# Kernel tuning notes

Hardware: AMD Instinct MI355X
Metric: run time of the kernel (lower is better)

Reference implementation:

```python
import jax, jax.numpy as jnp
import numpy as np

BN_EPS = 1e-5


def _conv_bn_elu(x, w, b, bn_scale, bn_bias, bn_mean, bn_var):
    # 1x1 conv == channel-mixing matmul: x [B,C,H,W], w [O,C]
    y = jnp.einsum('bchw,oc->bohw', x, w) + b[None, :, None, None]
    inv = bn_scale * jax.lax.rsqrt(bn_var + BN_EPS)
    y = y * inv[None, :, None, None] + (bn_bias - bn_mean * inv)[None, :, None, None]
    return jax.nn.elu(y)


def setup_inputs() -> dict:
    key = jax.random.key(0)
    ks = jax.random.split(key, 24)
    B, C, H, W = 4, 128, 64, 64
    d = {}
    d['x_q'] = jax.random.normal(ks[0], (B, C, H, W), jnp.float32)
    d['x_k'] = jax.random.normal(ks[1], (B, C, H, W), jnp.float32)
    d['x_v'] = jax.random.normal(ks[2], (B, C, H, W), jnp.float32)
    scale = 1.0 / np.sqrt(C)
    i = 3
    for p in ('q', 'k', 'v'):
        d[f'{p}_w'] = jax.random.normal(ks[i], (C, C), jnp.float32) * scale; i += 1
        d[f'{p}_b'] = jax.random.normal(ks[i], (C,), jnp.float32) * 0.01; i += 1
        d[f'{p}_bn_scale'] = jnp.ones((C,), jnp.float32) + 0.1 * jax.random.normal(ks[i], (C,), jnp.float32); i += 1
        d[f'{p}_bn_bias'] = 0.1 * jax.random.normal(ks[i], (C,), jnp.float32); i += 1
        d[f'{p}_bn_mean'] = 0.1 * jax.random.normal(ks[i], (C,), jnp.float32); i += 1
        d[f'{p}_bn_var'] = jax.random.uniform(ks[i], (C,), jnp.float32, 0.5, 1.5); i += 1
    # torch inits gamma/beta to zero; use small nonzero values so output is informative
    d['gamma'] = jnp.array([0.5], jnp.float32)
    d['beta'] = jnp.array([0.5], jnp.float32)
    return d


def reference(x_q, x_k, x_v,
              q_w, q_b, q_bn_scale, q_bn_bias, q_bn_mean, q_bn_var,
              k_w, k_b, k_bn_scale, k_bn_bias, k_bn_mean, k_bn_var,
              v_w, v_b, v_bn_scale, v_bn_bias, v_bn_mean, v_bn_var,
              gamma, beta):
    B, C, Hv, Wv = x_v.shape
    q = _conv_bn_elu(x_q, q_w, q_b, q_bn_scale, q_bn_bias, q_bn_mean, q_bn_var).reshape(B, C, -1)  # [B,C,HWq]
    k = _conv_bn_elu(x_k, k_w, k_b, k_bn_scale, k_bn_bias, k_bn_mean, k_bn_var).reshape(B, C, -1)  # [B,C,HWk]
    v = _conv_bn_elu(x_v, v_w, v_b, v_bn_scale, v_bn_bias, v_bn_mean, v_bn_var).reshape(B, C, -1)  # [B,C,HWv]
    energy = jnp.einsum('bcq,bck->bqk', q, k)                 # [B,HWq,HWk] (no scaling, as in source)
    attention = jax.nn.softmax(energy, axis=-1)
    out = jnp.einsum('bck,bqk->bcq', v, attention)            # [B,C,HWq]
    out = out.reshape(B, C, Hv, Wv)
    return gamma * out + beta * x_v
```

## Files before the change

kernel.cpp:

```cpp
#include <hip/hip_runtime.h>

#define CC 128
#define SS 4096
#define L2E 1.44269504f

typedef _Float16 f16;
typedef f16 f16x8 __attribute__((ext_vector_type(8)));
typedef float f32x4 __attribute__((ext_vector_type(4)));

struct PArg { const float *x, *w, *b, *sc, *bb, *bm, *bv; f16* out; };

__global__ __launch_bounds__(256) void projk(PArg A0, PArg A1, PArg A2) {
    const int p = blockIdx.y;
    PArg A = (p == 0) ? A0 : ((p == 1) ? A1 : A2);
    const int bx = blockIdx.x;
    const int b  = bx >> 6;
    const int s0 = (bx & 63) * 64;
    const int tid = threadIdx.x;
    const int w = tid >> 6, lane = tid & 63;
    const int n = lane & 15, g = lane >> 4;

    __shared__ f16 Xl[64][136];
    __shared__ f16 Wl[128][136];
    __shared__ float invA[128], ebA[128];
    f16* Yl = &Wl[0][0];

    if (tid < 128) {
        float iv = A.sc[tid] * rsqrtf(A.bv[tid] + 1e-5f);
        invA[tid] = iv;
        ebA[tid] = (A.b[tid] - A.bm[tid]) * iv + A.bb[tid];
    }
#pragma unroll
    for (int i = 0; i < 8; ++i) {
        int vi = tid + i * 256;
        int c = vi >> 4, sq = (vi & 15) * 4;
        float4 v = *(const float4*)(A.x + ((size_t)b * CC + c) * SS + s0 + sq);
        Xl[sq + 0][c] = (f16)v.x; Xl[sq + 1][c] = (f16)v.y;
        Xl[sq + 2][c] = (f16)v.z; Xl[sq + 3][c] = (f16)v.w;
    }
    __syncthreads();
#pragma unroll
    for (int i = 0; i < 8; ++i) {
        int vi = tid + i * 256;
        int o = vi >> 4, cq = (vi & 15) * 8;
        const float* wp = A.w + o * CC + cq;
        float4 a = *(const float4*)wp;
        float4 b4 = *(const float4*)(wp + 4);
        float iv = invA[o];
        union { f16 h[8]; uint4 u; } pk;
        pk.h[0] = (f16)(a.x * iv);  pk.h[1] = (f16)(a.y * iv);
        pk.h[2] = (f16)(a.z * iv);  pk.h[3] = (f16)(a.w * iv);
        pk.h[4] = (f16)(b4.x * iv); pk.h[5] = (f16)(b4.y * iv);
        pk.h[6] = (f16)(b4.z * iv); pk.h[7] = (f16)(b4.w * iv);
        *(uint4*)&Wl[o][cq] = pk.u;
    }
    __syncthreads();

    if (p < 2) {
        f32x4 acc[2][4];
#pragma unroll
        for (int mt = 0; mt < 2; ++mt)
#pragma unroll
            for (int nt = 0; nt < 4; ++nt) acc[mt][nt] = (f32x4){0.f, 0.f, 0.f, 0.f};
#pragma unroll
        for (int ks = 0; ks < 4; ++ks) {
            f16x8 af[2], bf[4];
#pragma unroll
            for (int mt = 0; mt < 2; ++mt) af[mt] = *(const f16x8*)&Wl[w * 32 + mt * 16 + n][ks * 32 + g * 8];
#pragma unroll
            for (int nt = 0; nt < 4; ++nt) bf[nt] = *(const f16x8*)&Xl[nt * 16 + n][ks * 32 + g * 8];
#pragma unroll
            for (int mt = 0; mt < 2; ++mt)
#pragma unroll
                for (int nt = 0; nt < 4; ++nt)
                    acc[mt][nt] = __builtin_amdgcn_mfma_f32_16x16x32_f16(af[mt], bf[nt], acc[mt][nt], 0, 0, 0);
        }
        __syncthreads();
#pragma unroll
        for (int mt = 0; mt < 2; ++mt) {
            float ebr[4];
#pragma unroll
            for (int r = 0; r < 4; ++r) ebr[r] = ebA[w * 32 + mt * 16 + g * 4 + r];
#pragma unroll
            for (int nt = 0; nt < 4; ++nt) {
                union { f16 h[4]; uint2 u; } pk;
#pragma unroll
                for (int r = 0; r < 4; ++r) {
                    float y = acc[mt][nt][r] + ebr[r];
                    y = (y > 0.f) ? y : (expf(y) - 1.f);
                    pk.h[r] = (f16)y;
                }
                *(uint2*)&Yl[(nt * 16 + n) * 136 + w * 32 + mt * 16 + g * 4] = pk.u;
            }
        }
        __syncthreads();
#pragma unroll
        for (int i = 0; i < 4; ++i) {
            int vi = tid + i * 256;
            int s = vi >> 4, cl = (vi & 15) * 8;
            *(uint4*)&A.out[((size_t)b * SS + s0 + s) * CC + cl] = *(const uint4*)&Yl[s * 136 + cl];
        }
    } else {
        f32x4 acc[8];
#pragma unroll
        for (int nt = 0; nt < 8; ++nt) acc[nt] = (f32x4){0.f, 0.f, 0.f, 0.f};
#pragma unroll
        for (int ks = 0; ks < 4; ++ks) {
            f16x8 af = *(const f16x8*)&Xl[w * 16 + n][ks * 32 + g * 8];
#pragma unroll
            for (int nt = 0; nt < 8; ++nt) {
                f16x8 bf = *(const f16x8*)&Wl[nt * 16 + n][ks * 32 + g * 8];
                acc[nt] = __builtin_amdgcn_mfma_f32_16x16x32_f16(af, bf, acc[nt], 0, 0, 0);
            }
        }
        __syncthreads();
#pragma unroll
        for (int nt = 0; nt < 8; ++nt) {
            float ebc = ebA[nt * 16 + n];
            union { f16 h[4]; uint2 u; } pk;
#pragma unroll
            for (int r = 0; r < 4; ++r) {
                float y = acc[nt][r] + ebc;
                y = (y > 0.f) ? y : (expf(y) - 1.f);
                pk.h[r] = (f16)y;
            }
            *(uint2*)&Yl[(nt * 16 + n) * 136 + w * 16 + g * 4] = pk.u;
        }
        __syncthreads();
#pragma unroll
        for (int i = 0; i < 4; ++i) {
            int vi = tid + i * 256;
            int o = vi >> 3, sl = (vi & 7) * 8;
            *(uint4*)&A.out[((size_t)b * CC + o) * SS + s0 + sl] = *(const uint4*)&Yl[o * 136 + sl];
        }
    }
}

__global__ __launch_bounds__(256, 3) void attnk(
    const f16* __restrict__ Qt, const f16* __restrict__ Kt, const f16* __restrict__ Vt,
    f16* __restrict__ Op, float* __restrict__ Ml)
{
    const int tid = threadIdx.x;
    const int bx = blockIdx.x;
    const int qt = bx & 31;
    const int kh = (bx >> 5) & 7;
    const int b  = bx >> 8;
    const int q0 = qt * 128;
    const int kbeg = kh * 512;

    __shared__ __align__(16) char arena[54272];
    f16 (*Kl)[136] = (f16(*)[136])arena;
    f16 (*Vl)[72]  = (f16(*)[72])(arena + 17408);

    const int w = tid >> 6, lane = tid & 63;
    const int n = lane & 15, g = lane >> 4;
    f16 (*Pw)[72] = (f16(*)[72])(arena + 35840 + w * 4608);

    f16x8 qf[2][4];
    {
        const f16* Qb = Qt + ((size_t)b * SS + q0 + w * 32) * CC;
#pragma unroll
        for (int qt2 = 0; qt2 < 2; ++qt2)
#pragma unroll
            for (int ks = 0; ks < 4; ++ks)
                qf[qt2][ks] = *(const f16x8*)&Qb[(qt2 * 16 + n) * CC + ks * 32 + g * 8];
    }

    f32x4 oacc[8][2];
#pragma unroll
    for (int mtc = 0; mtc < 8; ++mtc)
#pragma unroll
        for (int qt2 = 0; qt2 < 2; ++qt2) oacc[mtc][qt2] = (f32x4){0.f, 0.f, 0.f, 0.f};
    float mreg[2] = {-1e30f, -1e30f}, lsum[2] = {0.f, 0.f};

    for (int kt = 0; kt < 8; ++kt) {
        const int k0 = kbeg + kt * 64;
        __syncthreads();
#pragma unroll
        for (int i = 0; i < 4; ++i) {
            int vi = tid + i * 256;
            int rk = vi >> 4, ck = (vi & 15) * 8;
            *(uint4*)&Kl[rk][ck] = *(const uint4*)&Kt[((size_t)b * SS + k0 + rk) * CC + ck];
            int rv = vi >> 3, cv = (vi & 7) * 8;
            *(uint4*)&Vl[rv][cv] = *(const uint4*)&Vt[((size_t)b * CC + rv) * SS + k0 + cv];
        }
        __syncthreads();

        f32x4 sacc[4][2];
#pragma unroll
        for (int kt2 = 0; kt2 < 4; ++kt2)
#pragma unroll
            for (int qt2 = 0; qt2 < 2; ++qt2) sacc[kt2][qt2] = (f32x4){0.f, 0.f, 0.f, 0.f};
#pragma unroll
        for (int ks = 0; ks < 4; ++ks) {
            f16x8 kf[4];
#pragma unroll
            for (int kt2 = 0; kt2 < 4; ++kt2) kf[kt2] = *(const f16x8*)&Kl[kt2 * 16 + n][ks * 32 + g * 8];
#pragma unroll
            for (int kt2 = 0; kt2 < 4; ++kt2)
#pragma unroll
                for (int qt2 = 0; qt2 < 2; ++qt2)
                    sacc[kt2][qt2] = __builtin_amdgcn_mfma_f32_16x16x32_f16(kf[kt2], qf[qt2][ks], sacc[kt2][qt2], 0, 0, 0);
        }

        float al[2];
#pragma unroll
        for (int qt2 = 0; qt2 < 2; ++qt2) {
            float v = sacc[0][qt2][0];
#pragma unroll
            for (int kt2 = 0; kt2 < 4; ++kt2)
#pragma unroll
                for (int r = 0; r < 4; ++r) v = fmaxf(v, sacc[kt2][qt2][r]);
            v = fmaxf(v, __shfl_xor(v, 16));
            v = fmaxf(v, __shfl_xor(v, 32));
            float mn = fmaxf(mreg[qt2], v);
            al[qt2] = exp2f((mreg[qt2] - mn) * L2E);
            mreg[qt2] = mn;
            float rs = 0.f;
#pragma unroll
            for (int kt2 = 0; kt2 < 4; ++kt2) {
                union { f16 h[4]; uint2 u; } pk;
#pragma unroll
                for (int r = 0; r < 4; ++r) {
                    float p = exp2f((sacc[kt2][qt2][r] - mn) * L2E);
                    rs += p;
                    pk.h[r] = (f16)p;
                }
                *(uint2*)&Pw[qt2 * 16 + n][kt2 * 16 + g * 4] = pk.u;
            }
            lsum[qt2] = lsum[qt2] * al[qt2] + rs;
        }
#pragma unroll
        for (int mtc = 0; mtc < 8; ++mtc)
#pragma unroll
            for (int qt2 = 0; qt2 < 2; ++qt2)
#pragma unroll
                for (int r = 0; r < 4; ++r) oacc[mtc][qt2][r] *= al[qt2];

#pragma unroll
        for (int ks = 0; ks < 2; ++ks) {
            f16x8 vf[8], pf[2];
#pragma unroll
            for (int mtc = 0; mtc < 8; ++mtc) vf[mtc] = *(const f16x8*)&Vl[mtc * 16 + n][ks * 32 + g * 8];
#pragma unroll
            for (int qt2 = 0; qt2 < 2; ++qt2) pf[qt2] = *(const f16x8*)&Pw[qt2 * 16 + n][ks * 32 + g * 8];
#pragma unroll
            for (int mtc = 0; mtc < 8; ++mtc)
#pragma unroll
                for (int qt2 = 0; qt2 < 2; ++qt2)
                    oacc[mtc][qt2] = __builtin_amdgcn_mfma_f32_16x16x32_f16(vf[mtc], pf[qt2], oacc[mtc][qt2], 0, 0, 0);
        }
    }

    float lreg[2];
#pragma unroll
    for (int qt2 = 0; qt2 < 2; ++qt2) {
        float s = lsum[qt2];
        s += __shfl_xor(s, 16);
        s += __shfl_xor(s, 32);
        lreg[qt2] = s;
    }

    const int pidx = (b * 32 + qt) * 8 + kh;
    if (g == 0) {
        float* MlW = Ml + (size_t)pidx * 256;
#pragma unroll
        for (int qt2 = 0; qt2 < 2; ++qt2) {
            int q = w * 32 + qt2 * 16 + n;
            MlW[q]       = mreg[qt2];
            MlW[128 + q] = lreg[qt2];
        }
    }

    __syncthreads();
    f16 (*S2)[136] = (f16(*)[136])arena;
#pragma unroll
    for (int mtc = 0; mtc < 8; ++mtc)
#pragma unroll
        for (int qt2 = 0; qt2 < 2; ++qt2)
#pragma unroll
            for (int r = 0; r < 4; ++r)
                S2[mtc * 16 + g * 4 + r][w * 32 + qt2 * 16 + n] = (f16)oacc[mtc][qt2][r];
    __syncthreads();
    f16* OpW = Op + (size_t)pidx * 16384;
#pragma unroll
    for (int i = 0; i < 8; ++i) {
        int vi = tid + i * 256;
        int c = vi >> 4, qq = (vi & 15) * 8;
        *(uint4*)&OpW[c * 128 + qq] = *(const uint4*)&S2[c][qq];
    }
}

__global__ __launch_bounds__(256) void mrgk(
    const f16* __restrict__ Op, const float* __restrict__ Ml,
    const float* __restrict__ xv, const float* __restrict__ gp, const float* __restrict__ bp,
    float* __restrict__ out)
{
    const int bx = blockIdx.x;
    const int cg = bx & 3, bqt = bx >> 2;
    const int b = bqt >> 5, qt = bqt & 31;
    const int tid = threadIdx.x;
    const int q = tid & 127, hf = tid >> 7;

    const float* ml = Ml + (size_t)bqt * 8 * 256;
    float m = -1e30f;
#pragma unroll
    for (int k2 = 0; k2 < 8; ++k2) m = fmaxf(m, ml[k2 * 256 + q]);
    float wt[8], tot = 0.f;
#pragma unroll
    for (int k2 = 0; k2 < 8; ++k2) {
        wt[k2] = exp2f((ml[k2 * 256 + q] - m) * L2E);
        tot += wt[k2] * ml[k2 * 256 + 128 + q];
    }
    float inv = 1.f / tot;
    float gm = gp[0], bb = bp[0];

    const f16* O = Op + (size_t)bqt * 8 * 16384;
#pragma unroll 2
    for (int i = 0; i < 16; ++i) {
        int c = cg * 32 + hf * 16 + i;
        float o = 0.f;
#pragma unroll
        for (int k2 = 0; k2 < 8; ++k2) o += wt[k2] * (float)O[k2 * 16384 + c * 128 + q];
        o *= inv;
        size_t idx = ((size_t)(b * CC + c)) * SS + qt * 128 + q;
        out[idx] = gm * o + bb * xv[idx];
    }
}

extern "C" void kernel_launch(void* const* d_in, const int* in_sizes, int n_in,
                              void* d_out, int out_size, void* d_ws, size_t ws_size,
                              hipStream_t stream) {
    (void)in_sizes; (void)n_in; (void)out_size; (void)ws_size;

    const size_t TEN = (size_t)4 * SS * CC;
    f16* Qt = (f16*)d_ws;
    f16* Kt = Qt + TEN;
    f16* Vt = Kt + TEN;
    f16* Op = Vt + TEN;
    float* Ml = (float*)(Op + (size_t)1024 * 16384);

    PArg aq = { (const float*)d_in[0], (const float*)d_in[3],  (const float*)d_in[4],
                (const float*)d_in[5], (const float*)d_in[6],  (const float*)d_in[7],
                (const float*)d_in[8],  Qt };
    PArg ak = { (const float*)d_in[1], (const float*)d_in[9],  (const float*)d_in[10],
                (const float*)d_in[11], (const float*)d_in[12], (const float*)d_in[13],
                (const float*)d_in[14], Kt };
    PArg av = { (const float*)d_in[2], (const float*)d_in[15], (const float*)d_in[16],
                (const float*)d_in[17], (const float*)d_in[18], (const float*)d_in[19],
                (const float*)d_in[20], Vt };

    hipLaunchKernelGGL(projk, dim3(256, 3), dim3(256), 0, stream, aq, ak, av);
    hipLaunchKernelGGL(attnk, dim3(1024), dim3(256), 0, stream, Qt, Kt, Vt, Op, Ml);
    hipLaunchKernelGGL(mrgk, dim3(512), dim3(256), 0, stream,
                       Op, Ml, (const float*)d_in[2], (const float*)d_in[21],
                       (const float*)d_in[22], (float*)d_out);
}
```

Before: 215.9 us.

## Prefetch K/V tiles into registers, remap attention blocks, inline BN params

The attention kernel now loads the next K/V tile into registers while the current tile is computed, which hides global load latency at the cost of 32 extra VGPRs under a 3-waves occupancy bound. Its block index decomposition is reordered so that consecutive blocks share a query tile and batch across key halves, which changes L2 locality. The V fragment loads are interleaved with the MFMAs to lower register pressure. The projection kernel drops its shared BN-parameter arrays and one barrier by recomputing the scale and bias per thread from global memory, and uses fast __expf for ELU.

```diff
diff --git a/kernel.cpp b/kernel.cpp
--- a/kernel.cpp
+++ b/kernel.cpp
@@ -22,14 +22,8 @@
 
     __shared__ f16 Xl[64][136];
     __shared__ f16 Wl[128][136];
-    __shared__ float invA[128], ebA[128];
     f16* Yl = &Wl[0][0];
 
-    if (tid < 128) {
-        float iv = A.sc[tid] * rsqrtf(A.bv[tid] + 1e-5f);
-        invA[tid] = iv;
-        ebA[tid] = (A.b[tid] - A.bm[tid]) * iv + A.bb[tid];
-    }
 #pragma unroll
     for (int i = 0; i < 8; ++i) {
         int vi = tid + i * 256;
@@ -38,15 +32,14 @@
         Xl[sq + 0][c] = (f16)v.x; Xl[sq + 1][c] = (f16)v.y;
         Xl[sq + 2][c] = (f16)v.z; Xl[sq + 3][c] = (f16)v.w;
     }
-    __syncthreads();
 #pragma unroll
     for (int i = 0; i < 8; ++i) {
         int vi = tid + i * 256;
         int o = vi >> 4, cq = (vi & 15) * 8;
+        float iv = A.sc[o] * rsqrtf(A.bv[o] + 1e-5f);
         const float* wp = A.w + o * CC + cq;
         float4 a = *(const float4*)wp;
         float4 b4 = *(const float4*)(wp + 4);
-        float iv = invA[o];
         union { f16 h[8]; uint4 u; } pk;
         pk.h[0] = (f16)(a.x * iv);  pk.h[1] = (f16)(a.y * iv);
         pk.h[2] = (f16)(a.z * iv);  pk.h[3] = (f16)(a.w * iv);
@@ -80,14 +73,18 @@
         for (int mt = 0; mt < 2; ++mt) {
             float ebr[4];
 #pragma unroll
-            for (int r = 0; r < 4; ++r) ebr[r] = ebA[w * 32 + mt * 16 + g * 4 + r];
+            for (int r = 0; r < 4; ++r) {
+                int o = w * 32 + mt * 16 + g * 4 + r;
+                float iv = A.sc[o] * rsqrtf(A.bv[o] + 1e-5f);
+                ebr[r] = (A.b[o] - A.bm[o]) * iv + A.bb[o];
+            }
 #pragma unroll
             for (int nt = 0; nt < 4; ++nt) {
                 union { f16 h[4]; uint2 u; } pk;
 #pragma unroll
                 for (int r = 0; r < 4; ++r) {
                     float y = acc[mt][nt][r] + ebr[r];
-                    y = (y > 0.f) ? y : (expf(y) - 1.f);
+                    y = (y > 0.f) ? y : (__expf(y) - 1.f);
                     pk.h[r] = (f16)y;
                 }
                 *(uint2*)&Yl[(nt * 16 + n) * 136 + w * 32 + mt * 16 + g * 4] = pk.u;
@@ -116,12 +113,14 @@
         __syncthreads();
 #pragma unroll
         for (int nt = 0; nt < 8; ++nt) {
-            float ebc = ebA[nt * 16 + n];
+            int o = nt * 16 + n;
+            float iv = A.sc[o] * rsqrtf(A.bv[o] + 1e-5f);
+            float ebc = (A.b[o] - A.bm[o]) * iv + A.bb[o];
             union { f16 h[4]; uint2 u; } pk;
 #pragma unroll
             for (int r = 0; r < 4; ++r) {
                 float y = acc[nt][r] + ebc;
-                y = (y > 0.f) ? y : (expf(y) - 1.f);
+                y = (y > 0.f) ? y : (__expf(y) - 1.f);
                 pk.h[r] = (f16)y;
             }
             *(uint2*)&Yl[(nt * 16 + n) * 136 + w * 16 + g * 4] = pk.u;
@@ -142,9 +141,9 @@
 {
     const int tid = threadIdx.x;
     const int bx = blockIdx.x;
-    const int qt = bx & 31;
-    const int kh = (bx >> 5) & 7;
-    const int b  = bx >> 8;
+    const int kh = bx & 7;
+    const int b  = (bx >> 3) & 3;
+    const int qt = bx >> 5;
     const int q0 = qt * 128;
     const int kbeg = kh * 512;
 
@@ -173,6 +172,16 @@
         for (int qt2 = 0; qt2 < 2; ++qt2) oacc[mtc][qt2] = (f32x4){0.f, 0.f, 0.f, 0.f};
     float mreg[2] = {-1e30f, -1e30f}, lsum[2] = {0.f, 0.f};
 
+    uint4 pk4[4], pv4[4];
+#pragma unroll
+    for (int i = 0; i < 4; ++i) {
+        int vi = tid + i * 256;
+        int rk = vi >> 4, ck = (vi & 15) * 8;
+        pk4[i] = *(const uint4*)&Kt[((size_t)b * SS + kbeg + rk) * CC + ck];
+        int rv = vi >> 3, cv = (vi & 7) * 8;
+        pv4[i] = *(const uint4*)&Vt[((size_t)b * CC + rv) * SS + kbeg + cv];
+    }
+
     for (int kt = 0; kt < 8; ++kt) {
         const int k0 = kbeg + kt * 64;
         __syncthreads();
@@ -180,9 +189,19 @@
         for (int i = 0; i < 4; ++i) {
             int vi = tid + i * 256;
             int rk = vi >> 4, ck = (vi & 15) * 8;
-            *(uint4*)&Kl[rk][ck] = *(const uint4*)&Kt[((size_t)b * SS + k0 + rk) * CC + ck];
+            *(uint4*)&Kl[rk][ck] = pk4[i];
             int rv = vi >> 3, cv = (vi & 7) * 8;
-            *(uint4*)&Vl[rv][cv] = *(const uint4*)&Vt[((size_t)b * CC + rv) * SS + k0 + cv];
+            *(uint4*)&Vl[rv][cv] = pv4[i];
+        }
+        if (kt < 7) {
+#pragma unroll
+            for (int i = 0; i < 4; ++i) {
+                int vi = tid + i * 256;
+                int rk = vi >> 4, ck = (vi & 15) * 8;
+                pk4[i] = *(const uint4*)&Kt[((size_t)b * SS + k0 + 64 + rk) * CC + ck];
+                int rv = vi >> 3, cv = (vi & 7) * 8;
+                pv4[i] = *(const uint4*)&Vt[((size_t)b * CC + rv) * SS + k0 + 64 + cv];
+            }
         }
         __syncthreads();
 
@@ -239,16 +258,16 @@
 
 #pragma unroll
         for (int ks = 0; ks < 2; ++ks) {
-            f16x8 vf[8], pf[2];
-#pragma unroll
-            for (int mtc = 0; mtc < 8; ++mtc) vf[mtc] = *(const f16x8*)&Vl[mtc * 16 + n][ks * 32 + g * 8];
+            f16x8 pf[2];
 #pragma unroll
             for (int qt2 = 0; qt2 < 2; ++qt2) pf[qt2] = *(const f16x8*)&Pw[qt2 * 16 + n][ks * 32 + g * 8];
 #pragma unroll
-            for (int mtc = 0; mtc < 8; ++mtc)
+            for (int mtc = 0; mtc < 8; ++mtc) {
+                f16x8 vf = *(const f16x8*)&Vl[mtc * 16 + n][ks * 32 + g * 8];
 #pragma unroll
                 for (int qt2 = 0; qt2 < 2; ++qt2)
-                    oacc[mtc][qt2] = __builtin_amdgcn_mfma_f32_16x16x32_f16(vf[mtc], pf[qt2], oacc[mtc][qt2], 0, 0, 0);
+                    oacc[mtc][qt2] = __builtin_amdgcn_mfma_f32_16x16x32_f16(vf, pf[qt2], oacc[mtc][qt2], 0, 0, 0);
+            }
         }
     }
 
```

Result: slower. 276.7 us (+28.2%).
